# Kernel optimization log

Measured on AMD Instinct MI355X. Metric: run time of the kernel, lower is better.

## Reference

```python
import jax, jax.numpy as jnp
import numpy as np

B, T, D = 32, 1024, 1024  # batch, t_k (encoder steps), attn_sz == cell_state_sz


def setup_inputs() -> dict:
    key = jax.random.key(0)
    ks = jax.random.split(key, 7)
    scale = 1.0 / np.sqrt(D)
    return {
        "h_i": jax.random.normal(ks[0], (B, T, D), jnp.float32),
        "s_t": jax.random.normal(ks[1], (B, D), jnp.float32),
        "coverage": jax.random.uniform(ks[2], (B, T), jnp.float32),
        "W_h": jax.random.normal(ks[3], (D, D), jnp.float32) * scale,
        "W_s": jax.random.normal(ks[4], (D, D), jnp.float32) * scale,
        "b_s": jnp.zeros((D,), jnp.float32),
        "W_c": jax.random.normal(ks[5], (D,), jnp.float32) * scale,  # Dense(1 -> D) kernel
        "V_w": jax.random.normal(ks[6], (D,), jnp.float32) * scale,  # Dense(D -> 1) kernel
    }


def reference(h_i, s_t, coverage, W_h, W_s, b_s, W_c, V_w):
    # enc_features = W_h(h_i): (B, T, D)
    enc_features = jnp.einsum("btd,de->bte", h_i, W_h)
    # dec_features = W_s(s_t) broadcast over time: (B, 1, D)
    dec_features = (s_t @ W_s + b_s)[:, None, :]
    # coverage features: scalar coverage per step times (1->D) kernel
    cov_features = coverage[:, :, None] * W_c[None, None, :]
    features = enc_features + dec_features + cov_features
    # e_t = V(tanh(features)) squeezed to (B, T)
    e_t = jnp.einsum("btd,d->bt", jnp.tanh(features), V_w)
    a_t = jax.nn.softmax(e_t, axis=1)
    coverage_new = coverage + a_t
    # context = a_t @ h_i : (B, D)
    context_vector = jnp.einsum("bt,btd->bd", a_t, h_i)
    return context_vector, a_t, coverage_new
```

## Files before the change

### kernel.cpp

```cpp
#include <hip/hip_runtime.h>

#define B_ 32
#define T_ 1024
#define D_ 1024
#define M_ (B_ * T_)
#define NT_ 8
#define BM_ 128
#define BN_ 128
#define BK_ 64
#define NKT (D_ / BK_)
#define LSTR 72

#define FENCE_ALL() asm volatile("s_waitcnt vmcnt(0) lgkmcnt(0)" ::: "memory")

typedef __attribute__((ext_vector_type(8))) short short8;
typedef __attribute__((ext_vector_type(4))) float f32x4;

__device__ __forceinline__ unsigned f2bf(float f) {
    union { float f; unsigned u; } v; v.f = f;
    return (v.u + 0x7FFFu + ((v.u >> 16) & 1u)) >> 16;
}
__device__ __forceinline__ unsigned pack2(float a, float b) {
    return f2bf(a) | (f2bf(b) << 16);
}
__device__ __forceinline__ float bf2f(unsigned hi16) {
    union { unsigned u; float f; } v; v.u = hi16 << 16;
    return v.f;
}
__device__ __forceinline__ float fast_tanh(float x) {
    x = fminf(15.0f, fmaxf(-15.0f, x));
    float e = __expf(2.0f * x);
    return (e - 1.0f) * __fdividef(1.0f, e + 1.0f);
}

#define PREP_CONVH_BLKS 2048
#define PREP_CONVWT_BLKS 256
#define PREP_DEC_BLKS (B_ * 16)
__global__ __launch_bounds__(256) void prep_kernel(
    const float* __restrict__ h_i, uint4* __restrict__ h_bf4,
    const float* __restrict__ W_h, unsigned short* __restrict__ Wt,
    const float* __restrict__ s_t, const float* __restrict__ W_s,
    const float* __restrict__ b_s, float* __restrict__ dec_part)
{
    __shared__ float smem[64 * 65];
    const int bid = blockIdx.x;
    const int tid = threadIdx.x;
    if (bid < PREP_CONVH_BLKS) {
        const int idx = bid * 256 + tid;
        const int stride = PREP_CONVH_BLKS * 256;
        const int ngroups = M_ * D_ / 8;
        const float4* in4 = (const float4*)h_i;
        for (int g = idx; g < ngroups; g += stride) {
            const float4 a = in4[2 * g];
            const float4 b = in4[2 * g + 1];
            h_bf4[g] = make_uint4(pack2(a.x, a.y), pack2(a.z, a.w),
                                  pack2(b.x, b.y), pack2(b.z, b.w));
        }
    } else if (bid < PREP_CONVH_BLKS + PREP_CONVWT_BLKS) {
        const int tb = bid - PREP_CONVH_BLKS;
        float (*tile)[65] = (float (*)[65])smem;
        const int k0 = (tb & 15) * 64;
        const int n0 = (tb >> 4) * 64;
        const int tx = tid & 63, ty = tid >> 6;
#pragma unroll
        for (int r = 0; r < 16; ++r) {
            const int row = ty * 16 + r;
            tile[row][tx] = W_h[(size_t)(k0 + row) * D_ + n0 + tx];
        }
        __syncthreads();
#pragma unroll
        for (int r = 0; r < 16; ++r) {
            const int row = ty * 16 + r;
            Wt[(size_t)(n0 + row) * D_ + k0 + tx] = (unsigned short)f2bf(tile[tx][row]);
        }
    } else {
        const int db = bid - (PREP_CONVH_BLKS + PREP_CONVWT_BLKS);
        const int kc = db & 3;
        const int nc = (db >> 2) & 3;
        const int b  = db >> 4;
        const int d = nc * 256 + tid;
        const int k0 = kc * 256;
        float* s_lds = smem;
        s_lds[tid] = s_t[b * D_ + k0 + tid];
        __syncthreads();
        float acc = (kc == 0) ? b_s[d] : 0.f;
#pragma unroll 8
        for (int k = 0; k < 256; ++k) acc += s_lds[k] * W_s[(size_t)(k0 + k) * D_ + d];
        dec_part[kc * (B_ * D_) + b * D_ + d] = acc;
    }
}

__global__ __launch_bounds__(256, 2) void attn_gemm_fast(
    const unsigned short* __restrict__ h_bf, const unsigned short* __restrict__ wt_bf,
    const float* __restrict__ dec_part, const float* __restrict__ coverage,
    const float* __restrict__ W_c, const float* __restrict__ V_w,
    float* __restrict__ e_part)
{
    __shared__ __align__(16) unsigned short lA[BM_ * BK_];
    __shared__ __align__(16) unsigned short lB[BN_ * BK_];
    __shared__ float e_red[256];

    const int tid = threadIdx.x;
    const int mt = blockIdx.x >> 3;
    const int nt = blockIdx.x & 7;
    const int m0 = mt * BM_;
    const int n0 = nt * BN_;
    const int bb = m0 >> 10;

    const int wave = tid >> 6;
    const int lane = tid & 63;
    const int wr = wave >> 1, wc = wave & 1;
    const int lr = lane & 15;
    const int lk = lane >> 4;

    f32x4 acc[4][4];
    const f32x4 fzero = {0.f, 0.f, 0.f, 0.f};
#pragma unroll
    for (int i = 0; i < 4; ++i)
#pragma unroll
        for (int j = 0; j < 4; ++j) acc[i][j] = fzero;

    const char* gA = (const char*)h_bf + (size_t)m0 * (D_ * 2);
    const char* gB = (const char*)wt_bf + (size_t)n0 * (D_ * 2);
    const int lrow8 = lane >> 3;
    const int scol = (((lane & 7) ^ lrow8) << 4);

#define STAGE(k0)                                                                  \
    {                                                                              \
        _Pragma("unroll")                                                          \
        for (int j = 0; j < 4; ++j) {                                              \
            const int c = 4 * wave + j;                                            \
            const int row = c * 8 + lrow8;                                         \
            const size_t goff = (size_t)row * (D_ * 2) + (size_t)(k0) * 2 + scol;  \
            __builtin_amdgcn_global_load_lds(                                      \
                (const __attribute__((address_space(1))) void*)(gA + goff),        \
                (__attribute__((address_space(3))) void*)((char*)lA + c * 1024),   \
                16, 0, 0);                                                         \
            __builtin_amdgcn_global_load_lds(                                      \
                (const __attribute__((address_space(1))) void*)(gB + goff),        \
                (__attribute__((address_space(3))) void*)((char*)lB + c * 1024),   \
                16, 0, 0);                                                         \
        }                                                                          \
    }

    STAGE(0);
    const int sw = (lr & 7) << 4;

    for (int kt = 0; kt < NKT; ++kt) {
        FENCE_ALL();
        __syncthreads();

        short8 af[2][4], bfr[2][4];
#pragma unroll
        for (int kk = 0; kk < 2; ++kk)
#pragma unroll
            for (int i = 0; i < 4; ++i) {
                const int ar = wr * 64 + i * 16 + lr;
                const int br = wc * 64 + i * 16 + lr;
                const int kb = kk * 64 + lk * 16;
                af[kk][i]  = *(const short8*)((const char*)lA + ar * 128 + (kb ^ sw));
                bfr[kk][i] = *(const short8*)((const char*)lB + br * 128 + (kb ^ sw));
            }
        FENCE_ALL();
        __syncthreads();

        if (kt + 1 < NKT) STAGE((kt + 1) * BK_);

#pragma unroll
        for (int kk = 0; kk < 2; ++kk)
#pragma unroll
            for (int mi = 0; mi < 4; ++mi)
#pragma unroll
                for (int ni = 0; ni < 4; ++ni)
                    acc[mi][ni] = __builtin_amdgcn_mfma_f32_16x16x32_bf16(
                        af[kk][mi], bfr[kk][ni], acc[mi][ni], 0, 0, 0);
    }
#undef STAGE

    float esum[4][4];
    float covv[4][4];
#pragma unroll
    for (int mi = 0; mi < 4; ++mi)
#pragma unroll
        for (int r = 0; r < 4; ++r) {
            esum[mi][r] = 0.f;
            covv[mi][r] = coverage[m0 + wr * 64 + mi * 16 + lk * 4 + r];
        }
    const float* dp = dec_part + bb * D_;
#pragma unroll
    for (int ni = 0; ni < 4; ++ni) {
        const int n = n0 + wc * 64 + ni * 16 + lr;
        const float vw = V_w[n];
        const float dc = dp[n] + dp[B_ * D_ + n] + dp[2 * B_ * D_ + n] + dp[3 * B_ * D_ + n];
        const float wcv = W_c[n];
#pragma unroll
        for (int mi = 0; mi < 4; ++mi)
#pragma unroll
            for (int r = 0; r < 4; ++r) {
                const float f = acc[mi][ni][r] + dc + covv[mi][r] * wcv;
                esum[mi][r] += fast_tanh(f) * vw;
            }
    }
#pragma unroll
    for (int off = 1; off <= 8; off <<= 1)
#pragma unroll
        for (int mi = 0; mi < 4; ++mi)
#pragma unroll
            for (int r = 0; r < 4; ++r)
                esum[mi][r] += __shfl_xor(esum[mi][r], off, 64);

    if (lr == 0) {
#pragma unroll
        for (int mi = 0; mi < 4; ++mi)
#pragma unroll
            for (int r = 0; r < 4; ++r)
                e_red[wc * 128 + wr * 64 + mi * 16 + lk * 4 + r] = esum[mi][r];
    }
    FENCE_ALL();
    __syncthreads();
    if (tid < 128)
        e_part[(size_t)nt * M_ + m0 + tid] = e_red[tid] + e_red[128 + tid];
}

__global__ __launch_bounds__(256, 2) void attn_gemm_kernel(
    const float* __restrict__ h_i, const float* __restrict__ W_h,
    const float* __restrict__ dec_part, const float* __restrict__ coverage,
    const float* __restrict__ W_c, const float* __restrict__ V_w,
    float* __restrict__ e_part)
{
    __shared__ __align__(16) unsigned short lA[BM_][LSTR];
    __shared__ __align__(16) unsigned short lB[BN_][LSTR];
    __shared__ float e_red[256];

    const int tid = threadIdx.x;
    const int nt = blockIdx.x >> 8;
    const int mt = blockIdx.x & 255;
    const int m0 = mt * BM_;
    const int n0 = nt * BN_;
    const int bb = m0 >> 10;

    const int wave = tid >> 6;
    const int lane = tid & 63;
    const int wr = wave >> 1, wc = wave & 1;
    const int lr = lane & 15;
    const int lk = lane >> 4;

    f32x4 acc[4][4];
    const f32x4 fzero = {0.f, 0.f, 0.f, 0.f};
#pragma unroll
    for (int i = 0; i < 4; ++i)
#pragma unroll
        for (int j = 0; j < 4; ++j) acc[i][j] = fzero;

    const int a_row = tid >> 4;
    const int a_k = (tid & 15) << 2;
    const float* hA = h_i + (size_t)m0 * D_;

    for (int k0 = 0; k0 < D_; k0 += BK_) {
#pragma unroll
        for (int p = 0; p < 8; ++p) {
            const int row = a_row + p * 16;
            const float4 v = *(const float4*)(hA + (size_t)row * D_ + (k0 + a_k));
            *(uint2*)&lA[row][a_k] = make_uint2(pack2(v.x, v.y), pack2(v.z, v.w));
        }
#pragma unroll
        for (int p = 0; p < 8; ++p) {
            const int task = tid + p * 256;
            const int n = task & 127;
            const int kg = task >> 7;
            const float* wp = W_h + (size_t)(k0 + kg * 4) * D_ + n0 + n;
            const float x0 = wp[0 * D_], x1 = wp[1 * D_], x2 = wp[2 * D_], x3 = wp[3 * D_];
            *(uint2*)&lB[n][kg * 4] = make_uint2(pack2(x0, x1), pack2(x2, x3));
        }
        __syncthreads();

        short8 af[2][4], bfr[2][4];
#pragma unroll
        for (int kk = 0; kk < 2; ++kk)
#pragma unroll
            for (int i = 0; i < 4; ++i) {
                af[kk][i]  = *(const short8*)&lA[wr * 64 + i * 16 + lr][kk * 32 + lk * 8];
                bfr[kk][i] = *(const short8*)&lB[wc * 64 + i * 16 + lr][kk * 32 + lk * 8];
            }
#pragma unroll
        for (int kk = 0; kk < 2; ++kk)
#pragma unroll
            for (int mi = 0; mi < 4; ++mi)
#pragma unroll
                for (int ni = 0; ni < 4; ++ni)
                    acc[mi][ni] = __builtin_amdgcn_mfma_f32_16x16x32_bf16(
                        af[kk][mi], bfr[kk][ni], acc[mi][ni], 0, 0, 0);
        __syncthreads();
    }

    float esum[4][4];
    float covv[4][4];
#pragma unroll
    for (int mi = 0; mi < 4; ++mi)
#pragma unroll
        for (int r = 0; r < 4; ++r) {
            esum[mi][r] = 0.f;
            covv[mi][r] = coverage[m0 + wr * 64 + mi * 16 + lk * 4 + r];
        }
    const float* dp = dec_part + bb * D_;
#pragma unroll
    for (int ni = 0; ni < 4; ++ni) {
        const int n = n0 + wc * 64 + ni * 16 + lr;
        const float vw = V_w[n];
        const float dc = dp[n] + dp[B_ * D_ + n] + dp[2 * B_ * D_ + n] + dp[3 * B_ * D_ + n];
        const float wcv = W_c[n];
#pragma unroll
        for (int mi = 0; mi < 4; ++mi)
#pragma unroll
            for (int r = 0; r < 4; ++r) {
                const float f = acc[mi][ni][r] + dc + covv[mi][r] * wcv;
                esum[mi][r] += fast_tanh(f) * vw;
            }
    }
#pragma unroll
    for (int off = 1; off <= 8; off <<= 1)
#pragma unroll
        for (int mi = 0; mi < 4; ++mi)
#pragma unroll
            for (int r = 0; r < 4; ++r)
                esum[mi][r] += __shfl_xor(esum[mi][r], off, 64);

    if (lr == 0) {
#pragma unroll
        for (int mi = 0; mi < 4; ++mi)
#pragma unroll
            for (int r = 0; r < 4; ++r)
                e_red[wc * 128 + wr * 64 + mi * 16 + lk * 4 + r] = esum[mi][r];
    }
    __syncthreads();
    if (tid < 128)
        e_part[(size_t)nt * M_ + m0 + tid] = e_red[tid] + e_red[128 + tid];
}

__global__ __launch_bounds__(256) void softmax_kernel(
    const float* __restrict__ e_part, const float* __restrict__ coverage,
    float* __restrict__ a_out, float* __restrict__ cov_out,
    float* __restrict__ a_ws)
{
    const int b = blockIdx.x;
    const int tid = threadIdx.x;
    __shared__ float redmx[4], redsum[4];
    float e[4];
#pragma unroll
    for (int j = 0; j < 4; ++j) {
        const int t = tid + j * 256;
        float s = 0.f;
#pragma unroll
        for (int p = 0; p < NT_; ++p) s += e_part[(size_t)p * M_ + b * T_ + t];
        e[j] = s;
    }
    float mx = fmaxf(fmaxf(e[0], e[1]), fmaxf(e[2], e[3]));
#pragma unroll
    for (int off = 32; off > 0; off >>= 1) mx = fmaxf(mx, __shfl_xor(mx, off, 64));
    if ((tid & 63) == 0) redmx[tid >> 6] = mx;
    __syncthreads();
    mx = fmaxf(fmaxf(redmx[0], redmx[1]), fmaxf(redmx[2], redmx[3]));
    float p4[4];
    float ps = 0.f;
#pragma unroll
    for (int j = 0; j < 4; ++j) { p4[j] = __expf(e[j] - mx); ps += p4[j]; }
#pragma unroll
    for (int off = 32; off > 0; off >>= 1) ps += __shfl_xor(ps, off, 64);
    if ((tid & 63) == 0) redsum[tid >> 6] = ps;
    __syncthreads();
    ps = redsum[0] + redsum[1] + redsum[2] + redsum[3];
    const float inv = __fdividef(1.f, ps);
#pragma unroll
    for (int j = 0; j < 4; ++j) {
        const int idx = b * T_ + tid + j * 256;
        const float a = p4[j] * inv;
        a_out[idx] = a;
        a_ws[idx] = a;
        cov_out[idx] = coverage[idx] + a;
    }
}

__global__ __launch_bounds__(256) void ctx_part_bf(
    const unsigned short* __restrict__ h_bf, const float* __restrict__ a_t,
    float* __restrict__ ctx_part)
{
    const int bid = blockIdx.x;
    const int b = bid >> 3;
    const int dc = (bid >> 2) & 1;
    const int tc = bid & 3;
    const int tid = threadIdx.x;
    const int d0 = dc * 512 + tid * 2;
    __shared__ float a_lds[256];
    a_lds[tid] = a_t[b * T_ + tc * 256 + tid];
    __syncthreads();
    const unsigned short* hp = h_bf + ((size_t)(b * T_ + tc * 256)) * D_ + d0;
    float acc0 = 0.f, acc1 = 0.f;
#pragma unroll 8
    for (int t = 0; t < 256; ++t) {
        const unsigned v = *(const unsigned*)(hp + (size_t)t * D_);
        const float a = a_lds[t];
        acc0 += a * bf2f(v & 0xFFFFu);
        acc1 += a * bf2f(v >> 16);
    }
    *(float2*)(ctx_part + tc * (B_ * D_) + b * D_ + d0) = make_float2(acc0, acc1);
}

__global__ __launch_bounds__(256) void ctx_part_f32(
    const float* __restrict__ h_i, const float* __restrict__ a_t,
    float* __restrict__ ctx_part)
{
    const int bid = blockIdx.x;
    const int b = bid >> 4;
    const int dc = (bid >> 2) & 3;
    const int tc = bid & 3;
    const int tid = threadIdx.x;
    const int d = dc * 256 + tid;
    __shared__ float a_lds[256];
    a_lds[tid] = a_t[b * T_ + tc * 256 + tid];
    __syncthreads();
    const float* hp = h_i + ((size_t)(b * T_ + tc * 256)) * D_ + d;
    float acc = 0.f;
#pragma unroll 8
    for (int t = 0; t < 256; ++t) acc += a_lds[t] * hp[(size_t)t * D_];
    ctx_part[tc * (B_ * D_) + b * D_ + d] = acc;
}

__global__ __launch_bounds__(256) void dec_kernel(
    const float* __restrict__ s_t, const float* __restrict__ W_s,
    const float* __restrict__ b_s, float* __restrict__ dec_part)
{
    const int bid = blockIdx.x;
    const int kc = bid & 3;
    const int nc = (bid >> 2) & 3;
    const int b  = bid >> 4;
    const int d = nc * 256 + threadIdx.x;
    const int k0 = kc * 256;
    __shared__ float s_lds[256];
    s_lds[threadIdx.x] = s_t[b * D_ + k0 + threadIdx.x];
    __syncthreads();
    float acc = (kc == 0) ? b_s[d] : 0.f;
#pragma unroll 8
    for (int k = 0; k < 256; ++k) acc += s_lds[k] * W_s[(size_t)(k0 + k) * D_ + d];
    dec_part[kc * (B_ * D_) + b * D_ + d] = acc;
}

__global__ __launch_bounds__(256) void ctx_reduce_kernel(
    const float* __restrict__ ctx_part, float* __restrict__ out)
{
    const int i = blockIdx.x * 256 + threadIdx.x;
    out[i] = ctx_part[i] + ctx_part[B_ * D_ + i] + ctx_part[2 * B_ * D_ + i] +
             ctx_part[3 * B_ * D_ + i];
}

extern "C" void kernel_launch(void* const* d_in, const int* in_sizes, int n_in,
                              void* d_out, int out_size, void* d_ws, size_t ws_size,
                              hipStream_t stream)
{
    (void)in_sizes; (void)n_in; (void)out_size;
    const float* h_i      = (const float*)d_in[0];
    const float* s_t      = (const float*)d_in[1];
    const float* coverage = (const float*)d_in[2];
    const float* W_h      = (const float*)d_in[3];
    const float* W_s      = (const float*)d_in[4];
    const float* b_s      = (const float*)d_in[5];
    const float* W_c      = (const float*)d_in[6];
    const float* V_w      = (const float*)d_in[7];

    float* out     = (float*)d_out;
    float* ctx_out = out;
    float* a_out   = out + B_ * T_;
    float* cov_out = out + 2 * B_ * T_;

    float* ws       = (float*)d_ws;
    float* dec_part = ws;
    float* e_part   = dec_part + 4 * B_ * D_;
    float* ctx_part = e_part + NT_ * M_;
    float* a_ws     = ctx_part + 4 * B_ * D_;
    const size_t f32_count = 8 * (size_t)B_ * D_ + (size_t)NT_ * M_ + (size_t)B_ * T_;
    unsigned short* h_bf  = (unsigned short*)(ws + f32_count);
    unsigned short* wt_bf = h_bf + (size_t)M_ * D_;
    const size_t need = f32_count * 4 + ((size_t)M_ * D_ + (size_t)D_ * D_) * 2;

    if (ws_size >= need) {
        prep_kernel<<<PREP_CONVH_BLKS + PREP_CONVWT_BLKS + PREP_DEC_BLKS, 256, 0, stream>>>(
            h_i, (uint4*)h_bf, W_h, wt_bf, s_t, W_s, b_s, dec_part);
        attn_gemm_fast<<<NT_ * (M_ / BM_), 256, 0, stream>>>(h_bf, wt_bf, dec_part,
                                                             coverage, W_c, V_w, e_part);
        softmax_kernel<<<B_, 256, 0, stream>>>(e_part, coverage, a_out, cov_out, a_ws);
        ctx_part_bf<<<B_ * 8, 256, 0, stream>>>(h_bf, a_ws, ctx_part);
    } else {
        dec_kernel<<<B_ * 16, 256, 0, stream>>>(s_t, W_s, b_s, dec_part);
        attn_gemm_kernel<<<NT_ * (M_ / BM_), 256, 0, stream>>>(h_i, W_h, dec_part,
                                                               coverage, W_c, V_w, e_part);
        softmax_kernel<<<B_, 256, 0, stream>>>(e_part, coverage, a_out, cov_out, a_ws);
        ctx_part_f32<<<B_ * 16, 256, 0, stream>>>(h_i, a_ws, ctx_part);
    }
    ctx_reduce_kernel<<<(B_ * D_) / 256, 256, 0, stream>>>(ctx_part, ctx_out);
}
```

Measured before the change: 158.0 us.

## Enlarge attention GEMM tile to 256x256 with double-buffered LDS and phased MFMA

Result: slower. 161.3 us (+2.1%).

```diff
diff --git a/kernel.cpp b/kernel.cpp
--- a/kernel.cpp
+++ b/kernel.cpp
@@ -5,6 +5,7 @@
 #define D_ 1024
 #define M_ (B_ * T_)
 #define NT_ 8
+#define NT2 4
 #define BM_ 128
 #define BN_ 128
 #define BK_ 64
@@ -90,33 +91,33 @@
     }
 }
 
-__global__ __launch_bounds__(256, 2) void attn_gemm_fast(
+__global__ __launch_bounds__(512, 2) void attn_gemm2(
     const unsigned short* __restrict__ h_bf, const unsigned short* __restrict__ wt_bf,
     const float* __restrict__ dec_part, const float* __restrict__ coverage,
     const float* __restrict__ W_c, const float* __restrict__ V_w,
     float* __restrict__ e_part)
 {
-    __shared__ __align__(16) unsigned short lA[BM_ * BK_];
-    __shared__ __align__(16) unsigned short lB[BN_ * BK_];
-    __shared__ float e_red[256];
+    __shared__ __align__(16) unsigned short lds2[2][2][256 * 64];
+    __shared__ float e_red[4][256];
 
     const int tid = threadIdx.x;
-    const int mt = blockIdx.x >> 3;
-    const int nt = blockIdx.x & 7;
-    const int m0 = mt * BM_;
-    const int n0 = nt * BN_;
+    const int nt2 = blockIdx.x >> 7;
+    const int mt  = blockIdx.x & 127;
+    const int m0 = mt * 256;
+    const int n0 = nt2 * 256;
     const int bb = m0 >> 10;
 
     const int wave = tid >> 6;
     const int lane = tid & 63;
-    const int wr = wave >> 1, wc = wave & 1;
+    const int wr = wave >> 2;
+    const int wc = wave & 3;
     const int lr = lane & 15;
     const int lk = lane >> 4;
 
-    f32x4 acc[4][4];
+    f32x4 acc[8][4];
     const f32x4 fzero = {0.f, 0.f, 0.f, 0.f};
 #pragma unroll
-    for (int i = 0; i < 4; ++i)
+    for (int i = 0; i < 8; ++i)
 #pragma unroll
         for (int j = 0; j < 4; ++j) acc[i][j] = fzero;
 
@@ -124,67 +125,101 @@
     const char* gB = (const char*)wt_bf + (size_t)n0 * (D_ * 2);
     const int lrow8 = lane >> 3;
     const int scol = (((lane & 7) ^ lrow8) << 4);
-
-#define STAGE(k0)                                                                  \
+    const int sw = (lr & 7) << 4;
+
+#define STAGE2(buf, kt)                                                            \
     {                                                                              \
         _Pragma("unroll")                                                          \
         for (int j = 0; j < 4; ++j) {                                              \
-            const int c = 4 * wave + j;                                            \
+            const int c = wave * 4 + j;                                            \
             const int row = c * 8 + lrow8;                                         \
-            const size_t goff = (size_t)row * (D_ * 2) + (size_t)(k0) * 2 + scol;  \
+            const size_t goff = (size_t)row * (D_ * 2) + (size_t)(kt) * 128 + scol;\
             __builtin_amdgcn_global_load_lds(                                      \
                 (const __attribute__((address_space(1))) void*)(gA + goff),        \
-                (__attribute__((address_space(3))) void*)((char*)lA + c * 1024),   \
-                16, 0, 0);                                                         \
+                (__attribute__((address_space(3))) void*)((char*)lds2 +            \
+                    ((buf) * 2 + 0) * 32768 + c * 1024), 16, 0, 0);                \
             __builtin_amdgcn_global_load_lds(                                      \
                 (const __attribute__((address_space(1))) void*)(gB + goff),        \
-                (__attribute__((address_space(3))) void*)((char*)lB + c * 1024),   \
-                16, 0, 0);                                                         \
+                (__attribute__((address_space(3))) void*)((char*)lds2 +            \
+                    ((buf) * 2 + 1) * 32768 + c * 1024), 16, 0, 0);                \
         }                                                                          \
     }
 
-    STAGE(0);
-    const int sw = (lr & 7) << 4;
+    STAGE2(0, 0);
+    FENCE_ALL();
+    __syncthreads();
+
+    short8 aA[4][2];
+    short8 bB[4][2];
+
+#define LOADA(g)                                                                   \
+    _Pragma("unroll")                                                              \
+    for (int mi = 0; mi < 4; ++mi)                                                 \
+        _Pragma("unroll")                                                          \
+        for (int kk = 0; kk < 2; ++kk)                                             \
+            aA[mi][kk] = *(const short8*)(ldsA +                                   \
+                (wr * 128 + ((g) * 4 + mi) * 16 + lr) * 128 +                      \
+                (((kk) * 64 + lk * 16) ^ sw));
+
+#define LOADB(pair)                                                                \
+    _Pragma("unroll")                                                              \
+    for (int nn = 0; nn < 2; ++nn)                                                 \
+        _Pragma("unroll")                                                          \
+        for (int kk = 0; kk < 2; ++kk)                                             \
+            bB[(pair) * 2 + nn][kk] = *(const short8*)(ldsB +                      \
+                (wc * 64 + ((pair) * 2 + nn) * 16 + lr) * 128 +                    \
+                (((kk) * 64 + lk * 16) ^ sw));
+
+#define MFMA_Q(goff, npair)                                                        \
+    __builtin_amdgcn_s_setprio(1);                                                 \
+    _Pragma("unroll")                                                              \
+    for (int mi = 0; mi < 4; ++mi)                                                 \
+        _Pragma("unroll")                                                          \
+        for (int nn = 0; nn < 2; ++nn)                                             \
+            _Pragma("unroll")                                                      \
+            for (int kk = 0; kk < 2; ++kk)                                         \
+                acc[(goff) + mi][(npair) * 2 + nn] =                               \
+                    __builtin_amdgcn_mfma_f32_16x16x32_bf16(                       \
+                        aA[mi][kk], bB[(npair) * 2 + nn][kk],                      \
+                        acc[(goff) + mi][(npair) * 2 + nn], 0, 0, 0);              \
+    __builtin_amdgcn_s_setprio(0);
 
     for (int kt = 0; kt < NKT; ++kt) {
+        const int cur = kt & 1;
+        const char* ldsA = (const char*)lds2 + (cur * 2 + 0) * 32768;
+        const char* ldsB = (const char*)lds2 + (cur * 2 + 1) * 32768;
+
+        if (kt + 1 < NKT) STAGE2(cur ^ 1, kt + 1);
+        LOADA(0);
+        LOADB(0);
+        MFMA_Q(0, 0);
+        __builtin_amdgcn_s_barrier();
+
+        LOADB(1);
+        MFMA_Q(0, 1);
+        __builtin_amdgcn_s_barrier();
+
+        LOADA(1);
+        MFMA_Q(4, 1);
+        __builtin_amdgcn_s_barrier();
+
+        MFMA_Q(4, 0);
         FENCE_ALL();
         __syncthreads();
-
-        short8 af[2][4], bfr[2][4];
-#pragma unroll
-        for (int kk = 0; kk < 2; ++kk)
-#pragma unroll
-            for (int i = 0; i < 4; ++i) {
-                const int ar = wr * 64 + i * 16 + lr;
-                const int br = wc * 64 + i * 16 + lr;
-                const int kb = kk * 64 + lk * 16;
-                af[kk][i]  = *(const short8*)((const char*)lA + ar * 128 + (kb ^ sw));
-                bfr[kk][i] = *(const short8*)((const char*)lB + br * 128 + (kb ^ sw));
-            }
-        FENCE_ALL();
-        __syncthreads();
-
-        if (kt + 1 < NKT) STAGE((kt + 1) * BK_);
-
-#pragma unroll
-        for (int kk = 0; kk < 2; ++kk)
-#pragma unroll
-            for (int mi = 0; mi < 4; ++mi)
-#pragma unroll
-                for (int ni = 0; ni < 4; ++ni)
-                    acc[mi][ni] = __builtin_amdgcn_mfma_f32_16x16x32_bf16(
-                        af[kk][mi], bfr[kk][ni], acc[mi][ni], 0, 0, 0);
-    }
-#undef STAGE
-
-    float esum[4][4];
-    float covv[4][4];
-#pragma unroll
-    for (int mi = 0; mi < 4; ++mi)
+    }
+#undef STAGE2
+#undef LOADA
+#undef LOADB
+#undef MFMA_Q
+
+    float esum[8][4];
+    float covv[8][4];
+#pragma unroll
+    for (int mi = 0; mi < 8; ++mi)
 #pragma unroll
         for (int r = 0; r < 4; ++r) {
             esum[mi][r] = 0.f;
-            covv[mi][r] = coverage[m0 + wr * 64 + mi * 16 + lk * 4 + r];
+            covv[mi][r] = coverage[m0 + wr * 128 + mi * 16 + lk * 4 + r];
         }
     const float* dp = dec_part + bb * D_;
 #pragma unroll
@@ -194,7 +229,7 @@
         const float dc = dp[n] + dp[B_ * D_ + n] + dp[2 * B_ * D_ + n] + dp[3 * B_ * D_ + n];
         const float wcv = W_c[n];
 #pragma unroll
-        for (int mi = 0; mi < 4; ++mi)
+        for (int mi = 0; mi < 8; ++mi)
 #pragma unroll
             for (int r = 0; r < 4; ++r) {
                 const float f = acc[mi][ni][r] + dc + covv[mi][r] * wcv;
@@ -204,22 +239,23 @@
 #pragma unroll
     for (int off = 1; off <= 8; off <<= 1)
 #pragma unroll
-        for (int mi = 0; mi < 4; ++mi)
+        for (int mi = 0; mi < 8; ++mi)
 #pragma unroll
             for (int r = 0; r < 4; ++r)
                 esum[mi][r] += __shfl_xor(esum[mi][r], off, 64);
 
     if (lr == 0) {
 #pragma unroll
-        for (int mi = 0; mi < 4; ++mi)
+        for (int mi = 0; mi < 8; ++mi)
 #pragma unroll
             for (int r = 0; r < 4; ++r)
-                e_red[wc * 128 + wr * 64 + mi * 16 + lk * 4 + r] = esum[mi][r];
+                e_red[wc][wr * 128 + mi * 16 + lk * 4 + r] = esum[mi][r];
     }
     FENCE_ALL();
     __syncthreads();
-    if (tid < 128)
-        e_part[(size_t)nt * M_ + m0 + tid] = e_red[tid] + e_red[128 + tid];
+    if (tid < 256)
+        e_part[(size_t)nt2 * M_ + m0 + tid] =
+            e_red[0][tid] + e_red[1][tid] + e_red[2][tid] + e_red[3][tid];
 }
 
 __global__ __launch_bounds__(256, 2) void attn_gemm_kernel(
@@ -340,7 +376,7 @@
 __global__ __launch_bounds__(256) void softmax_kernel(
     const float* __restrict__ e_part, const float* __restrict__ coverage,
     float* __restrict__ a_out, float* __restrict__ cov_out,
-    float* __restrict__ a_ws)
+    float* __restrict__ a_ws, int nparts)
 {
     const int b = blockIdx.x;
     const int tid = threadIdx.x;
@@ -350,8 +386,7 @@
     for (int j = 0; j < 4; ++j) {
         const int t = tid + j * 256;
         float s = 0.f;
-#pragma unroll
-        for (int p = 0; p < NT_; ++p) s += e_part[(size_t)p * M_ + b * T_ + t];
+        for (int p = 0; p < nparts; ++p) s += e_part[(size_t)p * M_ + b * T_ + t];
         e[j] = s;
     }
     float mx = fmaxf(fmaxf(e[0], e[1]), fmaxf(e[2], e[3]));
@@ -484,15 +519,15 @@
     if (ws_size >= need) {
         prep_kernel<<<PREP_CONVH_BLKS + PREP_CONVWT_BLKS + PREP_DEC_BLKS, 256, 0, stream>>>(
             h_i, (uint4*)h_bf, W_h, wt_bf, s_t, W_s, b_s, dec_part);
-        attn_gemm_fast<<<NT_ * (M_ / BM_), 256, 0, stream>>>(h_bf, wt_bf, dec_part,
-                                                             coverage, W_c, V_w, e_part);
-        softmax_kernel<<<B_, 256, 0, stream>>>(e_part, coverage, a_out, cov_out, a_ws);
+        attn_gemm2<<<NT2 * (M_ / 256), 512, 0, stream>>>(h_bf, wt_bf, dec_part,
+                                                         coverage, W_c, V_w, e_part);
+        softmax_kernel<<<B_, 256, 0, stream>>>(e_part, coverage, a_out, cov_out, a_ws, NT2);
         ctx_part_bf<<<B_ * 8, 256, 0, stream>>>(h_bf, a_ws, ctx_part);
     } else {
         dec_kernel<<<B_ * 16, 256, 0, stream>>>(s_t, W_s, b_s, dec_part);
         attn_gemm_kernel<<<NT_ * (M_ / BM_), 256, 0, stream>>>(h_i, W_h, dec_part,
                                                                coverage, W_c, V_w, e_part);
-        softmax_kernel<<<B_, 256, 0, stream>>>(e_part, coverage, a_out, cov_out, a_ws);
+        softmax_kernel<<<B_, 256, 0, stream>>>(e_part, coverage, a_out, cov_out, a_ws, NT_);
         ctx_part_f32<<<B_ * 16, 256, 0, stream>>>(h_i, a_ws, ctx_part);
     }
     ctx_reduce_kernel<<<(B_ * D_) / 256, 256, 0, stream>>>(ctx_part, ctx_out);
```
